# Kernel optimization log

Measured on AMD Instinct MI355X. Metric: run time of the kernel, lower is better.

Reference implementation:

```python
import jax, jax.numpy as jnp
import numpy as np

H = 32        # num attention heads
KVH = 8       # num key/value heads
HD = 64       # head dim
D = H * HD    # hidden size 2048
EPS = 1e-6
ROPE_THETA = 10000.0
MAX_POS = 2048


def rotate_half(x):
    x1, x2 = jnp.split(x, 2, axis=-1)
    return jnp.concatenate((-x2, x1), axis=-1)


def rms_norm(x, w):
    # per-head RMSNorm over last dim, computed in fp32 like the torch module
    x32 = x.astype(jnp.float32)
    inv = jax.lax.rsqrt(jnp.mean(x32 * x32, axis=-1, keepdims=True) + EPS)
    return w * (x32 * inv).astype(x.dtype)


def setup_inputs() -> dict:
    key = jax.random.key(0)
    ks = jax.random.split(key, 6)
    B, S = 2, 2048
    hidden_states = jax.random.normal(ks[0], (B, S, D), dtype=jnp.float32)
    # rotary tables [MAX_POS, HD]
    inv_freq = 1.0 / (ROPE_THETA ** (np.arange(0, HD, 2, dtype=np.float32) / HD))
    t = np.arange(MAX_POS, dtype=np.float32)
    freqs = np.outer(t, inv_freq)                      # [MAX_POS, HD/2]
    emb = np.concatenate([freqs, freqs], axis=-1)      # [MAX_POS, HD]
    cos = jnp.asarray(np.cos(emb))
    sin = jnp.asarray(np.sin(emb))
    scale = 1.0 / np.sqrt(D)
    wq = jax.random.normal(ks[1], (D, D), dtype=jnp.float32) * scale
    wk = jax.random.normal(ks[2], (D, KVH * HD), dtype=jnp.float32) * scale
    wv = jax.random.normal(ks[3], (D, KVH * HD), dtype=jnp.float32) * scale
    wo = jax.random.normal(ks[4], (D, D), dtype=jnp.float32) * scale
    q_ln_w = jnp.ones((HD,), dtype=jnp.float32)
    k_ln_w = jnp.ones((HD,), dtype=jnp.float32)
    return {"hidden_states": hidden_states, "cos": cos, "sin": sin,
            "wq": wq, "wk": wk, "wv": wv, "wo": wo,
            "q_ln_w": q_ln_w, "k_ln_w": k_ln_w}


def reference(hidden_states, cos, sin, wq, wk, wv, wo, q_ln_w, k_ln_w):
    B, S, _ = hidden_states.shape
    n_rep = H // KVH
    q = (hidden_states @ wq).reshape(B, S, H, HD)
    k = (hidden_states @ wk).reshape(B, S, KVH, HD)
    v = (hidden_states @ wv).reshape(B, S, KVH, HD)
    # per-head RMSNorm on q/k, then to (B, heads, S, HD)
    q = rms_norm(q, q_ln_w).transpose(0, 2, 1, 3)
    k = rms_norm(k, k_ln_w).transpose(0, 2, 1, 3)
    v = v.transpose(0, 2, 1, 3)
    # RoPE
    c = cos[:S][None, None]  # [1,1,S,HD]
    s = sin[:S][None, None]
    q = q * c + rotate_half(q) * s
    k = k * c + rotate_half(k) * s
    # GQA: repeat kv heads
    k = jnp.repeat(k, n_rep, axis=1)
    v = jnp.repeat(v, n_rep, axis=1)
    scores = jnp.einsum('bhqd,bhkd->bhqk', q, k) / np.sqrt(HD)
    causal = jnp.tril(jnp.ones((S, S), dtype=bool))
    scores = jnp.where(causal, scores, -jnp.inf)
    p = jax.nn.softmax(scores.astype(jnp.float32), axis=-1).astype(q.dtype)
    out = jnp.einsum('bhqk,bhkd->bhqd', p, v)
    out = out.transpose(0, 2, 1, 3).reshape(B, S, D)
    return out @ wo
```

## Files before the change

### kernel.cpp

```cpp
#include <hip/hip_runtime.h>
#include <hip/hip_bf16.h>

#define HH 32
#define KVHN 8
#define HD 64
#define DMODEL 2048
#define SEQ 2048
#define BB 2
#define NTOK 4096
#define DKV 512
#define NQKV 3072

typedef __bf16 bf16x8 __attribute__((ext_vector_type(8)));
typedef __bf16 bf16x4 __attribute__((ext_vector_type(4)));
typedef float  f32x4  __attribute__((ext_vector_type(4)));

typedef const __attribute__((address_space(1))) void gvoid_t;
typedef __attribute__((address_space(3))) void lvoid_t;

__device__ inline void glds16(const void* g, void* l) {
  __builtin_amdgcn_global_load_lds((gvoid_t*)g, (lvoid_t*)l, 16, 0, 0);
}

__device__ inline f32x4 mfma16(bf16x8 a, bf16x8 b, f32x4 c) {
  return __builtin_amdgcn_mfma_f32_16x16x32_bf16(a, b, c, 0, 0, 0);
}

__device__ inline float fast_exp2(float x) {
  float r;
  asm("v_exp_f32 %0, %1" : "=v"(r) : "v"(x));
  return r;
}


__global__ __launch_bounds__(256)
void k_cvt_hidden(const float* __restrict__ in, __bf16* __restrict__ out) {
  int i = (blockIdx.x * 256 + threadIdx.x) * 4;
  f32x4 v = *(const f32x4*)(in + i);
  bf16x4 o;
  o[0] = (__bf16)v[0]; o[1] = (__bf16)v[1]; o[2] = (__bf16)v[2]; o[3] = (__bf16)v[3];
  *(bf16x4*)(out + i) = o;
}

__global__ __launch_bounds__(256)
void k_transpose_w(const float* __restrict__ W, __bf16* __restrict__ T, int K, int N) {
  __shared__ float tile[32][33];
  int n0 = blockIdx.x * 32, k0 = blockIdx.y * 32;
  int tx = threadIdx.x & 31, ty = threadIdx.x >> 5;
#pragma unroll
  for (int i = 0; i < 32; i += 8)
    tile[ty + i][tx] = W[(size_t)(k0 + ty + i) * N + n0 + tx];
  __syncthreads();
#pragma unroll
  for (int i = 0; i < 32; i += 8)
    T[(size_t)(n0 + ty + i) * K + k0 + tx] = (__bf16)tile[tx][ty + i];
}

__global__ __launch_bounds__(256)
void k_transpose_kv(const float* __restrict__ WK, const float* __restrict__ WV,
                    __bf16* __restrict__ T) {
  __shared__ float tile[32][33];
  const float* W = blockIdx.z ? WV : WK;
  __bf16* Td = T + (size_t)(2048 + blockIdx.z * 512) * 2048;
  int n0 = blockIdx.x * 32, k0 = blockIdx.y * 32;
  int tx = threadIdx.x & 31, ty = threadIdx.x >> 5;
#pragma unroll
  for (int i = 0; i < 32; i += 8)
    tile[ty + i][tx] = W[(size_t)(k0 + ty + i) * 512 + n0 + tx];
  __syncthreads();
#pragma unroll
  for (int i = 0; i < 32; i += 8)
    Td[(size_t)(n0 + ty + i) * 2048 + k0 + tx] = (__bf16)tile[tx][ty + i];
}

__global__ __launch_bounds__(256)
void k_transpose_v(const __bf16* __restrict__ Vt, __bf16* __restrict__ VT) {
  __shared__ __bf16 tile[32][33];
  int c0 = blockIdx.x * 32, s0 = blockIdx.y * 32, b = blockIdx.z;
  int tx = threadIdx.x & 31, ty = threadIdx.x >> 5;
#pragma unroll
  for (int i = 0; i < 32; i += 8)
    tile[ty + i][tx] = Vt[(size_t)(b * SEQ + s0 + ty + i) * DKV + c0 + tx];
  __syncthreads();
#pragma unroll
  for (int i = 0; i < 32; i += 8)
    VT[(size_t)(b * DKV + c0 + ty + i) * SEQ + s0 + tx] = tile[tx][ty + i];
}


__device__ inline void stc(float* p, float v)  { *p = v; }
__device__ inline void stc(__bf16* p, float v) { *p = (__bf16)v; }

template <int EPI, typename CT>
__global__ __launch_bounds__(256, 4)
void k_gemm3(const __bf16* __restrict__ A, const __bf16* __restrict__ BT,
             CT* __restrict__ C, int M, int N, int K,
             const float* __restrict__ cosT, const float* __restrict__ sinT,
             const float* __restrict__ qw, const float* __restrict__ kw,
             __bf16* __restrict__ Qr, __bf16* __restrict__ Kr,
             __bf16* __restrict__ Vt) {
  __shared__ alignas(16) __bf16 Al[2][128 * 32];
  __shared__ alignas(16) __bf16 Bl[2][128 * 32];
  const int tid = threadIdx.x;
  const int wid = tid >> 6, lane = tid & 63, g = lane >> 4, r16 = lane & 15;
  const int wm = wid >> 1, wn = wid & 1;
  const int nbm = M >> 7, nbn = N >> 7;
  const int nwg = nbm * nbn;
  int id = blockIdx.x;
  id = (id & 7) * (nwg >> 3) + (id >> 3);
  const int bm = id % nbm, bn = id / nbm;

  const int sr1 = tid >> 2, sr2 = 64 + (tid >> 2);
  const int c1 = (((tid & 3) ^ (sr1 & 3) ^ ((sr1 >> 2) & 3))) * 8;
  const int c2 = (((tid & 3) ^ (sr2 & 3) ^ ((sr2 >> 2) & 3))) * 8;
  const __bf16* gA1 = A + (size_t)(bm * 128 + sr1) * K + c1;
  const __bf16* gA2 = A + (size_t)(bm * 128 + sr2) * K + c2;
  const __bf16* gB1 = BT + (size_t)(bn * 128 + sr1) * K + c1;
  const __bf16* gB2 = BT + (size_t)(bn * 128 + sr2) * K + c2;

  int aoff[4], boff[4];
#pragma unroll
  for (int m = 0; m < 4; ++m) {
    int row = wm * 64 + m * 16 + r16;
    aoff[m] = row * 32 + (g ^ (row & 3) ^ ((row >> 2) & 3)) * 8;
  }
#pragma unroll
  for (int n = 0; n < 4; ++n) {
    int row = wn * 64 + n * 16 + r16;
    boff[n] = row * 32 + (g ^ (row & 3) ^ ((row >> 2) & 3)) * 8;
  }

  auto STAGE = [&](int sl, int kt) {
    const int ko = kt * 32;
    glds16(gA1 + ko, &Al[sl][tid * 8]);
    glds16(gA2 + ko, &Al[sl][2048 + tid * 8]);
    glds16(gB1 + ko, &Bl[sl][tid * 8]);
    glds16(gB2 + ko, &Bl[sl][2048 + tid * 8]);
  };

  f32x4 acc[4][4] = {};
  const int nk = K >> 5;

  STAGE(0, 0);
  for (int kt = 0; kt < nk; ++kt) {
    const int s = kt & 1;
    if (kt + 1 < nk) {
      STAGE(s ^ 1, kt + 1);
      asm volatile("s_waitcnt vmcnt(4)" ::: "memory");
    } else {
      asm volatile("s_waitcnt vmcnt(0)" ::: "memory");
    }
    __builtin_amdgcn_s_barrier();
    bf16x8 af[4], bfr[4];
#pragma unroll
    for (int m = 0; m < 4; ++m) af[m] = *(const bf16x8*)&Al[s][aoff[m]];
#pragma unroll
    for (int n = 0; n < 4; ++n) bfr[n] = *(const bf16x8*)&Bl[s][boff[n]];
    __builtin_amdgcn_s_setprio(1);
#pragma unroll
    for (int m = 0; m < 4; ++m)
#pragma unroll
      for (int n = 0; n < 4; ++n)
        acc[m][n] = mfma16(af[m], bfr[n], acc[m][n]);
    __builtin_amdgcn_s_setprio(0);
    __builtin_amdgcn_s_barrier();
  }

  if (EPI == 0) {
#pragma unroll
    for (int m = 0; m < 4; ++m) {
      int row = bm * 128 + wm * 64 + m * 16 + g * 4;
#pragma unroll
      for (int n = 0; n < 4; ++n) {
        int col = bn * 128 + wn * 64 + n * 16 + r16;
#pragma unroll
        for (int r = 0; r < 4; ++r)
          stc(&C[(size_t)(row + r) * N + col], acc[m][n][r]);
      }
    }
  } else {
    const int colbase = bn * 128 + wn * 64;
    const float QSCALE = 0.18033688011112042f;
    if (colbase < DMODEL + DKV) {
      const bool isq = colbase < DMODEL;
      const float* wp = isq ? qw : kw;
      const float qs = isq ? QSCALE : 1.0f;
      float w4[4];
#pragma unroll
      for (int n = 0; n < 4; ++n) w4[n] = wp[n * 16 + r16];
#pragma unroll
      for (int m = 0; m < 4; ++m) {
        const int rowm = bm * 128 + wm * 64 + m * 16 + g * 4;
        float ss[4];
#pragma unroll
        for (int r = 0; r < 4; ++r) {
          ss[r] = acc[m][0][r] * acc[m][0][r] + acc[m][1][r] * acc[m][1][r] +
                  acc[m][2][r] * acc[m][2][r] + acc[m][3][r] * acc[m][3][r];
#pragma unroll
          for (int mk = 1; mk < 16; mk <<= 1) ss[r] += __shfl_xor(ss[r], mk);
          ss[r] = rsqrtf(ss[r] * (1.0f / HD) + 1e-6f);
        }
#pragma unroll
        for (int r = 0; r < 4; ++r) {
          const int t = rowm + r;
          const int sidx = t & (SEQ - 1);
          const float inv_ = ss[r];
#pragma unroll
          for (int n = 0; n < 4; ++n) {
            const int d = n * 16 + r16;
            const float xn = acc[m][n][r] * inv_ * w4[n];
            const float xp = acc[m][n ^ 2][r] * inv_ * w4[n ^ 2];
            const float rot = (n < 2) ? -xp : xp;
            const float cv = cosT[sidx * HD + d], sv = sinT[sidx * HD + d];
            const float o = (xn * cv + rot * sv) * qs;
            if (isq) {
              const int hq = colbase >> 6;
              Qr[((size_t)t * HH + hq) * HD + d] = (__bf16)o;
            } else {
              const int kvh = (colbase - DMODEL) >> 6;
              Kr[((size_t)t * KVHN + kvh) * HD + d] = (__bf16)o;
            }
          }
        }
      }
    } else {
      const int vc0 = colbase - (DMODEL + DKV);
#pragma unroll
      for (int m = 0; m < 4; ++m) {
        const int rowm = bm * 128 + wm * 64 + m * 16 + g * 4;
#pragma unroll
        for (int n = 0; n < 4; ++n)
#pragma unroll
          for (int r = 0; r < 4; ++r)
            Vt[(size_t)(rowm + r) * DKV + vc0 + n * 16 + r16] = (__bf16)acc[m][n][r];
      }
    }
  }
}


__global__ __launch_bounds__(512)
void k_attn(const __bf16* __restrict__ Q, const __bf16* __restrict__ Kg,
            const __bf16* __restrict__ VT, __bf16* __restrict__ O) {
  __shared__ alignas(16) __bf16 Kl[2][64 * 64];
  __shared__ alignas(16) __bf16 Vl[2][64 * 64];
  __shared__ alignas(16) __bf16 Pl[8][16 * 72];
  const int f = blockIdx.x;
  const int b = f >> 8;
  const int h = (f & 255) >> 3;
  const int j = f & 7;
  const int kvh = h >> 2;
  const int tid = threadIdx.x, wid = tid >> 6, lane = tid & 63;
  const int g = lane >> 4, r16 = lane & 15;
  __bf16* Pw = Pl[wid];

  const int rr = lane >> 3;
  const int cc = (lane & 7) ^ rr;

  auto STAGE = [&](int buf, int kb) {
    const int krow = kb * 64 + wid * 8 + rr;
    glds16(&Kg[((size_t)(b * SEQ + krow) * KVHN + kvh) * HD + cc * 8],
           &Kl[buf][wid * 512]);
    const int d = wid * 8 + rr;
    glds16(&VT[(size_t)(b * DKV + kvh * HD + d) * SEQ + (size_t)kb * 64 + cc * 8],
           &Vl[buf][wid * 512]);
  };

#pragma unroll 1
  for (int phase = 0; phase < 2; ++phase) {
    const int qt = phase ? j : 15 - j;
    const int q0 = qt * 128 + wid * 16;
    const int ntile = 2 * qt + 2;

    bf16x8 qf[2];
#pragma unroll
    for (int h2 = 0; h2 < 2; ++h2)
      qf[h2] = *(const bf16x8*)&Q[(((size_t)b * SEQ + q0 + r16) * HH + h) * HD + h2 * 32 + g * 8];

    f32x4 acc[4] = {};
    float l_p[4] = {};

    STAGE(0, 0);
    asm volatile("s_waitcnt vmcnt(0)" ::: "memory");
    __syncthreads();

    for (int kb = 0; kb < ntile; ++kb) {
      const int cur = kb & 1;
      if (kb + 1 < ntile) STAGE(cur ^ 1, kb + 1);
      const __bf16* Kb = Kl[cur];
      const __bf16* Vb = Vl[cur];
      if (kb * 64 <= q0 + 15) {
        bf16x8 kf[4][2];
#pragma unroll
        for (int ks = 0; ks < 4; ++ks)
#pragma unroll
          for (int h2 = 0; h2 < 2; ++h2) {
            const int p = r16 + ks * 16;
            const int ch = (g + 4 * h2) ^ (p & 7);
            kf[ks][h2] = *(const bf16x8*)&Kb[p * 64 + ch * 8];
          }
        const bool needmask = (kb * 64 + 63 > q0);
        float svv[4][4];
        __builtin_amdgcn_s_setprio(1);
#pragma unroll
        for (int ks = 0; ks < 4; ++ks) {
          f32x4 sacc = {-12.f, -12.f, -12.f, -12.f};
          sacc = mfma16(qf[0], kf[ks][0], sacc);
          sacc = mfma16(qf[1], kf[ks][1], sacc);
#pragma unroll
          for (int r = 0; r < 4; ++r) svv[ks][r] = sacc[r];
        }
        __builtin_amdgcn_s_setprio(0);
        if (needmask) {
#pragma unroll
          for (int ks = 0; ks < 4; ++ks)
#pragma unroll
            for (int r = 0; r < 4; ++r) {
              int pg = kb * 64 + ks * 16 + r16;
              int qg = q0 + g * 4 + r;
              if (pg > qg) svv[ks][r] = -1e30f;
            }
        }
#pragma unroll
        for (int ks = 0; ks < 4; ++ks)
#pragma unroll
          for (int r = 0; r < 4; ++r) {
            float p = fast_exp2(svv[ks][r]);
            l_p[r] += p;
            Pw[(g * 4 + r) * 72 + ks * 16 + r16] = (__bf16)p;
          }
        bf16x8 pf0 = *(const bf16x8*)&Pw[r16 * 72 + g * 8];
        bf16x8 pf1 = *(const bf16x8*)&Pw[r16 * 72 + 32 + g * 8];
        __builtin_amdgcn_s_setprio(1);
#pragma unroll
        for (int nb = 0; nb < 4; ++nb) {
          const int d = r16 + nb * 16;
          const int ch0 = g ^ (d & 7), ch1 = (4 + g) ^ (d & 7);
          bf16x8 vf0 = *(const bf16x8*)&Vb[d * 64 + ch0 * 8];
          bf16x8 vf1 = *(const bf16x8*)&Vb[d * 64 + ch1 * 8];
          acc[nb] = mfma16(pf0, vf0, acc[nb]);
          acc[nb] = mfma16(pf1, vf1, acc[nb]);
        }
        __builtin_amdgcn_s_setprio(0);
      }
      asm volatile("s_waitcnt vmcnt(0)" ::: "memory");
      __syncthreads();
    }
#pragma unroll
    for (int mk = 1; mk < 16; mk <<= 1)
#pragma unroll
      for (int r = 0; r < 4; ++r) l_p[r] += __shfl_xor(l_p[r], mk);
    float inv[4];
#pragma unroll
    for (int r = 0; r < 4; ++r) inv[r] = 1.0f / l_p[r];
#pragma unroll
    for (int nb = 0; nb < 4; ++nb)
#pragma unroll
      for (int r = 0; r < 4; ++r)
        O[(((size_t)b * SEQ + q0 + g * 4 + r) * HH + h) * HD + nb * 16 + r16] =
            (__bf16)(acc[nb][r] * inv[r]);
  }
}


extern "C" void kernel_launch(void* const* d_in, const int* in_sizes, int n_in,
                              void* d_out, int out_size, void* d_ws, size_t ws_size,
                              hipStream_t stream) {
  const float* hidden = (const float*)d_in[0];
  const float* cosT   = (const float*)d_in[1];
  const float* sinT   = (const float*)d_in[2];
  const float* wq     = (const float*)d_in[3];
  const float* wk     = (const float*)d_in[4];
  const float* wv     = (const float*)d_in[5];
  const float* wo     = (const float*)d_in[6];
  const float* qw     = (const float*)d_in[7];
  const float* kw     = (const float*)d_in[8];
  float* out = (float*)d_out;
  char* ws = (char*)d_ws;

  __bf16* Abf  = (__bf16*)(ws);
  __bf16* Ob   = Abf;
  __bf16* WT   = (__bf16*)(ws + (16u << 20));
  __bf16* Qr   = (__bf16*)(ws + (28u << 20));
  __bf16* Kr   = (__bf16*)(ws + (44u << 20));
  __bf16* Vtmp = (__bf16*)(ws + (48u << 20));
  __bf16* VT   = (__bf16*)(ws + (52u << 20));
  __bf16* WoT  = (__bf16*)(ws + (56u << 20));

  k_cvt_hidden<<<8192, 256, 0, stream>>>(hidden, Abf);
  k_transpose_w<<<dim3(64, 64), 256, 0, stream>>>(wq, WT, 2048, 2048);
  k_transpose_kv<<<dim3(16, 64, 2), 256, 0, stream>>>(wk, wv, WT);
  k_transpose_w<<<dim3(64, 64), 256, 0, stream>>>(wo, WoT, 2048, 2048);

  k_gemm3<1, __bf16><<<768, 256, 0, stream>>>(Abf, WT, (__bf16*)nullptr,
      NTOK, NQKV, DMODEL, cosT, sinT, qw, kw, Qr, Kr, Vtmp);

  k_transpose_v<<<dim3(16, 64, 2), 256, 0, stream>>>(Vtmp, VT);

  k_attn<<<dim3(512), 512, 0, stream>>>(Qr, Kr, VT, Ob);

  k_gemm3<0, float><<<512, 256, 0, stream>>>(Ob, WoT, out,
      NTOK, DMODEL, DMODEL, nullptr, nullptr, nullptr, nullptr,
      nullptr, nullptr, nullptr);
}
```

Baseline: 201.9 us.

## Use 256x256-tile 8-wave GEMM with interleaved prefetch for QKV projection

Adds a new GEMM kernel with 256x256 output tiles, 512 threads and software-pipelined LDS loads interleaved with MFMA phases, and uses it for the fused QKV projection with its RMSNorm/RoPE epilogue. The larger tile raises operand reuse per LDS byte and lowers global traffic. In exchange it launches only 192 blocks, fewer than the CU count, and uses more registers and LDS per block.

```diff
diff --git a/kernel.cpp b/kernel.cpp
--- a/kernel.cpp
+++ b/kernel.cpp
@@ -178,8 +178,118 @@
           stc(&C[(size_t)(row + r) * N + col], acc[m][n][r]);
       }
     }
+  }
+}
+
+
+template <int EPI, typename CT>
+__global__ __launch_bounds__(512, 2)
+void k_gemm8(const __bf16* __restrict__ A, const __bf16* __restrict__ BT,
+             CT* __restrict__ C, int M, int N, int K,
+             const float* __restrict__ cosT, const float* __restrict__ sinT,
+             const float* __restrict__ qw, const float* __restrict__ kw,
+             __bf16* __restrict__ Qr, __bf16* __restrict__ Kr,
+             __bf16* __restrict__ Vt) {
+  __shared__ alignas(16) __bf16 Al[2][256 * 64];
+  __shared__ alignas(16) __bf16 Bl[2][256 * 64];
+  const int tid = threadIdx.x;
+  const int wid = tid >> 6, lane = tid & 63, g = lane >> 4, r16 = lane & 15;
+  const int wm = wid >> 2, wn = wid & 3;
+  const int nbm = M >> 8, nbn = N >> 8;
+  const int nwg = nbm * nbn;
+  int id = blockIdx.x;
+  id = (id & 7) * (nwg >> 3) + (id >> 3);
+  const int bm = id % nbm, bn = id / nbm;
+
+  const int srow = tid >> 3;
+  const int schunk = tid & 7;
+  const int sc = (schunk ^ (srow & 7)) * 8;
+  const __bf16* gA = A + (size_t)(bm * 256 + srow) * K + sc;
+  const __bf16* gB = BT + (size_t)(bn * 256 + srow) * K + sc;
+
+  auto SA = [&](int buf, int kt, int q) {
+    glds16(gA + (size_t)q * 64 * K + kt * 64,
+           &Al[buf][(q * 64 + srow) * 64 + schunk * 8]);
+  };
+  auto SB = [&](int buf, int kt, int q) {
+    glds16(gB + (size_t)q * 64 * K + kt * 64,
+           &Bl[buf][(q * 64 + srow) * 64 + schunk * 8]);
+  };
+
+  const int cs0 = (g ^ (r16 & 7)) * 8;
+  const int cs1 = ((4 + g) ^ (r16 & 7)) * 8;
+
+  f32x4 acc[8][4] = {};
+  const int nk = K >> 6;
+
+  SB(0, 0, 0); SB(0, 0, 1); SB(0, 0, 2); SB(0, 0, 3);
+  SA(0, 0, 0); SA(0, 0, 1); SA(0, 0, 2); SA(0, 0, 3);
+  SB(1, 1, 0); SB(1, 1, 1); SB(1, 1, 2); SB(1, 1, 3);
+  asm volatile("s_waitcnt vmcnt(4)" ::: "memory");
+  __builtin_amdgcn_s_barrier();
+
+#pragma unroll 1
+  for (int t = 0; t < nk; ++t) {
+    const int cur = t & 1;
+    const __bf16* Ab = Al[cur];
+    const __bf16* Bb = Bl[cur];
+    const bool pfA = (t + 1 < nk), pfB = (t + 2 < nk);
+    bf16x8 bfr[4][2];
+#pragma unroll
+    for (int p = 0; p < 4; ++p) {
+      bf16x8 af[2][2];
+#pragma unroll
+      for (int j = 0; j < 2; ++j) {
+        const int row = wm * 128 + (2 * p + j) * 16 + r16;
+        af[j][0] = *(const bf16x8*)&Ab[row * 64 + cs0];
+        af[j][1] = *(const bf16x8*)&Ab[row * 64 + cs1];
+      }
+      if (p == 0) {
+#pragma unroll
+        for (int n = 0; n < 4; ++n) {
+          const int row = wn * 64 + n * 16 + r16;
+          bfr[n][0] = *(const bf16x8*)&Bb[row * 64 + cs0];
+          bfr[n][1] = *(const bf16x8*)&Bb[row * 64 + cs1];
+        }
+      }
+      asm volatile("" ::: "memory");
+      if (p < 2) {
+        if (pfA) { SA(cur ^ 1, t + 1, 2 * p); SA(cur ^ 1, t + 1, 2 * p + 1); }
+      } else {
+        if (pfB) { SB(cur, t + 2, 2 * (p - 2)); SB(cur, t + 2, 2 * p - 3); }
+      }
+      if (p == 3) {
+        if (pfB) asm volatile("s_waitcnt vmcnt(4)" ::: "memory");
+        else     asm volatile("s_waitcnt vmcnt(0)" ::: "memory");
+      }
+      __builtin_amdgcn_s_barrier();
+      __builtin_amdgcn_s_setprio(1);
+#pragma unroll
+      for (int j = 0; j < 2; ++j)
+#pragma unroll
+        for (int n = 0; n < 4; ++n) {
+          acc[2 * p + j][n] = mfma16(af[j][0], bfr[n][0], acc[2 * p + j][n]);
+          acc[2 * p + j][n] = mfma16(af[j][1], bfr[n][1], acc[2 * p + j][n]);
+        }
+      __builtin_amdgcn_s_setprio(0);
+      __builtin_amdgcn_s_barrier();
+    }
+  }
+
+  if (EPI == 0) {
+#pragma unroll
+    for (int m = 0; m < 8; ++m) {
+      int row = bm * 256 + wm * 128 + m * 16 + g * 4;
+#pragma unroll
+      for (int n = 0; n < 4; ++n) {
+        int col = bn * 256 + wn * 64 + n * 16 + r16;
+#pragma unroll
+        for (int r = 0; r < 4; ++r)
+          stc(&C[(size_t)(row + r) * N + col], acc[m][n][r]);
+      }
+    }
   } else {
-    const int colbase = bn * 128 + wn * 64;
+    const int colbase = bn * 256 + wn * 64;
     const float QSCALE = 0.18033688011112042f;
     if (colbase < DMODEL + DKV) {
       const bool isq = colbase < DMODEL;
@@ -189,8 +299,8 @@
 #pragma unroll
       for (int n = 0; n < 4; ++n) w4[n] = wp[n * 16 + r16];
 #pragma unroll
-      for (int m = 0; m < 4; ++m) {
-        const int rowm = bm * 128 + wm * 64 + m * 16 + g * 4;
+      for (int m = 0; m < 8; ++m) {
+        const int rowm = bm * 256 + wm * 128 + m * 16 + g * 4;
         float ss[4];
 #pragma unroll
         for (int r = 0; r < 4; ++r) {
@@ -226,8 +336,8 @@
     } else {
       const int vc0 = colbase - (DMODEL + DKV);
 #pragma unroll
-      for (int m = 0; m < 4; ++m) {
-        const int rowm = bm * 128 + wm * 64 + m * 16 + g * 4;
+      for (int m = 0; m < 8; ++m) {
+        const int rowm = bm * 256 + wm * 128 + m * 16 + g * 4;
 #pragma unroll
         for (int n = 0; n < 4; ++n)
 #pragma unroll
@@ -392,7 +502,7 @@
   k_transpose_kv<<<dim3(16, 64, 2), 256, 0, stream>>>(wk, wv, WT);
   k_transpose_w<<<dim3(64, 64), 256, 0, stream>>>(wo, WoT, 2048, 2048);
 
-  k_gemm3<1, __bf16><<<768, 256, 0, stream>>>(Abf, WT, (__bf16*)nullptr,
+  k_gemm8<1, __bf16><<<192, 512, 0, stream>>>(Abf, WT, (__bf16*)nullptr,
       NTOK, NQKV, DMODEL, cosT, sinT, qw, kw, Qr, Kr, Vtmp);
 
   k_transpose_v<<<dim3(16, 64, 2), 256, 0, stream>>>(Vtmp, VT);
```

New measurement: 203.4 us. About the same (+0.7%).
